# Optimization experiments

Measured on AMD Instinct MI355X. Metric: run time of the kernel, lower is better.

The kernel has to match this reference:

```python
import jax, jax.numpy as jnp
import numpy as np
import math

N_HEAD = 8
LN_EPS = 1e-5


def _layernorm(x, g, b):
    mu = jnp.mean(x, axis=-1, keepdims=True)
    var = jnp.mean(jnp.square(x - mu), axis=-1, keepdims=True)
    return (x - mu) / jnp.sqrt(var + LN_EPS) * g + b


def setup_inputs() -> dict:
    key0 = jax.random.key(0)
    ks = jax.random.split(key0, 12)
    B, L, D, E = 4, 512, 256, 5  # batch, agents, n_embd, edge_feats_dim

    def w(k, shape):
        return jax.random.normal(k, shape, dtype=jnp.float32) * 0.02

    return {
        "key": jax.random.normal(ks[0], (B, L, D), jnp.float32),
        "value": jax.random.normal(ks[1], (B, L, D), jnp.float32),
        "query": jax.random.normal(ks[2], (B, L, D), jnp.float32),
        "atten_masks": jax.random.randint(ks[3], (B, L, L), 0, 2).astype(jnp.int32),
        "edge_feats": jax.random.normal(ks[4], (B, L, L, E), jnp.float32),
        # Linear weights stored [in, out] so forward is x @ W + b
        "Wk": w(ks[5], (D, D)), "bk": jnp.zeros((D,), jnp.float32),
        "Wq": w(ks[6], (D, D)), "bq": jnp.zeros((D,), jnp.float32),
        "Wv": w(ks[7], (D, D)), "bv": jnp.zeros((D,), jnp.float32),
        "Wp": w(ks[8], (D, D)), "bp": jnp.zeros((D,), jnp.float32),
        "We1": w(ks[9], (E, D)), "be1": jnp.zeros((D,), jnp.float32),
        "ln_g": jnp.ones((D,), jnp.float32), "ln_b": jnp.zeros((D,), jnp.float32),
        "We2": w(ks[10], (D, N_HEAD)), "be2": jnp.zeros((N_HEAD,), jnp.float32),
    }


def reference(key, value, query, atten_masks, edge_feats,
              Wk, bk, Wq, bq, Wv, bv, Wp, bp,
              We1, be1, ln_g, ln_b, We2, be2):
    B, L, D = query.shape
    hd = D // N_HEAD
    # QKV projections -> [B, H, L, hd]
    q = (query @ Wq + bq).reshape(B, L, N_HEAD, hd).transpose(0, 2, 1, 3)
    k = (key @ Wk + bk).reshape(B, L, N_HEAD, hd).transpose(0, 2, 1, 3)
    v = (value @ Wv + bv).reshape(B, L, N_HEAD, hd).transpose(0, 2, 1, 3)
    # scaled attention scores [B, H, L, L]
    att = jnp.einsum('bhqd,bhkd->bhqk', q, k) * (1.0 / math.sqrt(hd))
    # edge-feature additive bias: Linear -> ReLU -> LayerNorm -> Linear(per-head)
    e = jax.nn.relu(edge_feats @ We1 + be1)          # [B, L, L, D]
    e = _layernorm(e, ln_g, ln_b)
    e = e @ We2 + be2                                # [B, L, L, H]
    att = att + e.transpose(0, 3, 1, 2)
    # additive mask (0 -> -inf), softmax over keys
    att = jnp.where(atten_masks[:, None, :, :] == 0, -jnp.inf, att)
    att = jax.nn.softmax(att, axis=-1)
    y = jnp.einsum('bhqk,bhkd->bhqd', att, v)        # [B, H, L, hd]
    y = y.transpose(0, 2, 1, 3).reshape(B, L, D)
    return y @ Wp + bp
```

## Files before the change

kernel.cpp:

```cpp
#include <hip/hip_runtime.h>
#include <hip/hip_bf16.h>

#define L_SEQ 512
#define D_EMB 256
#define NH 8
#define HD 32
#define LL (L_SEQ * L_SEQ)

typedef __attribute__((ext_vector_type(8))) short short8;
typedef __attribute__((ext_vector_type(4))) float f32x4;
typedef unsigned short ushort;

__device__ __forceinline__ float bf2f(ushort u) {
    unsigned int x = ((unsigned int)u) << 16;
    float f;
    __builtin_memcpy(&f, &x, 4);
    return f;
}
__device__ __forceinline__ ushort f2bf(float x) {
    __hip_bfloat16 h = __float2bfloat16(x);
    ushort u;
    __builtin_memcpy(&u, &h, 2);
    return u;
}
__device__ __forceinline__ unsigned int fbits(float x) {
    unsigned int u;
    __builtin_memcpy(&u, &x, 4);
    return u;
}
__device__ __forceinline__ float asf(unsigned int u) {
    float f;
    __builtin_memcpy(&f, &u, 4);
    return f;
}
__device__ __forceinline__ unsigned int pack_bf16rnd(float a, float b) {
    return __builtin_amdgcn_perm(fbits(b) + 0x8000u, fbits(a) + 0x8000u, 0x07060302u);
}
__device__ __forceinline__ unsigned int packhi(unsigned int y, unsigned int x) {
    return __builtin_amdgcn_perm(y, x, 0x07060302u);
}
__device__ __forceinline__ uint2 cvt_hilo2(float v0, float v1) {
    unsigned int hi = pack_bf16rnd(v0, v1);
    float h0 = asf(hi << 16);
    float h1 = asf(hi & 0xffff0000u);
    unsigned int lo = pack_bf16rnd(v0 - h0, v1 - h1);
    uint2 r; r.x = hi; r.y = lo;
    return r;
}

__global__ __launch_bounds__(256) void prep_kernel(
    const float* __restrict__ We1, const float* __restrict__ be1,
    const float* __restrict__ g,   const float* __restrict__ bta,
    const float* __restrict__ We2, const float* __restrict__ be2,
    const float* __restrict__ Wq, const float* __restrict__ Wk,
    const float* __restrict__ Wv, const float* __restrict__ Wp,
    ushort* __restrict__ W1G, ushort* __restrict__ B2G, float* __restrict__ tail,
    ushort* __restrict__ WThi, ushort* __restrict__ WTlo)
{
    int t = threadIdx.x;
    if (blockIdx.x != 0) {
        int bx = blockIdx.x - 1;
        int w = bx >> 4, ny = bx & 15;
        const float* W = (w == 0) ? Wq : (w == 1) ? Wk : (w == 2) ? Wv : Wp;
        ushort* dh = WThi + (size_t)w * 65536;
        ushort* dl = WTlo + (size_t)w * 65536;
        int n = ny * 16 + (t >> 4);
        int k0 = (t & 15) * 16;
        ushort hbuf[16], lbuf[16];
#pragma unroll
        for (int kk = 0; kk < 16; ++kk) {
            float v = W[(size_t)(k0 + kk) * 256 + n];
            unsigned int hb = fbits(v) + 0x8000u;
            ushort hi = (ushort)(hb >> 16);
            float res = v - bf2f(hi);
            hbuf[kk] = hi;
            lbuf[kk] = (ushort)((fbits(res) + 0x8000u) >> 16);
        }
        *(short8*)(dh + (size_t)n * 256 + k0)     = *(short8*)&hbuf[0];
        *(short8*)(dh + (size_t)n * 256 + k0 + 8) = *(short8*)&hbuf[8];
        *(short8*)(dl + (size_t)n * 256 + k0)     = *(short8*)&lbuf[0];
        *(short8*)(dl + (size_t)n * 256 + k0 + 8) = *(short8*)&lbuf[8];
        return;
    }

    __shared__ float red[16][256];
    float gd = g[t], bd = bta[t];
#pragma unroll
    for (int h = 0; h < 8; ++h) {
        float w2 = We2[t * 8 + h];
        red[h][t] = gd * w2;
        red[8 + h][t] = bd * w2;
    }
    __syncthreads();
    for (int off = 128; off > 0; off >>= 1) {
        if (t < off) {
#pragma unroll
            for (int row = 0; row < 16; ++row) red[row][t] += red[row][t + off];
        }
        __syncthreads();
    }
    if (t < 8) {
        tail[t] = red[t][0];
        tail[8 + t] = red[8 + t][0] + be2[t];
    }
    if (t >= 16 && t < 32) tail[t] = 0.f;

    for (int idx = t; idx < 8192; idx += 256) {
        int j = idx & 7, lane = (idx >> 3) & 63, tile = idx >> 9;
        int m = lane & 15, q = lane >> 4;
        int k = q * 8 + j;
        int d = (m >> 2) * 64 + tile * 4 + (m & 3);
        float v = 0.f;
        bool lo = false;
        if (k < 5)        v = We1[k * 256 + d];
        else if (k < 10)  { v = We1[(k - 5) * 256 + d]; lo = true; }
        else if (k < 15)  v = We1[(k - 10) * 256 + d];
        else if (k == 15) v = be1[d];
        else if (k == 16) { v = be1[d]; lo = true; }
        ushort hi = f2bf(v);
        W1G[idx] = lo ? f2bf(v - bf2f(hi)) : hi;
    }
    for (int idx = t; idx < 4096; idx += 256) {
        int j = idx & 7, lane = (idx >> 3) & 63, kc = idx >> 9;
        int n = lane & 15, q = lane >> 4;
        int d = kc * 32 + q * 8 + j;
        ushort out;
        if (n < 8)       out = f2bf(g[d] * We2[d * 8 + n]);
        else if (n == 8) out = 0x3F80;
        else             out = 0;
        B2G[idx] = out;
    }
}

__global__ __launch_bounds__(256) void gemm_mfma(
    const float* __restrict__ A0, const ushort* __restrict__ H0,
    const ushort* __restrict__ L0, const float* __restrict__ b0,
    float* __restrict__ C0, float* __restrict__ T0,
    const float* __restrict__ A1, const ushort* __restrict__ H1,
    const ushort* __restrict__ L1, const float* __restrict__ b1,
    float* __restrict__ C1, float* __restrict__ T1,
    const float* __restrict__ A2, const ushort* __restrict__ H2,
    const ushort* __restrict__ L2, const float* __restrict__ b2,
    float* __restrict__ C2, float* __restrict__ T2)
{
    const float* A; const ushort* BH; const ushort* BL;
    const float* bias; float* C; float* Ct;
    if (blockIdx.z == 0)      { A = A0; BH = H0; BL = L0; bias = b0; C = C0; Ct = T0; }
    else if (blockIdx.z == 1) { A = A1; BH = H1; BL = L1; bias = b1; C = C1; Ct = T1; }
    else                      { A = A2; BH = H2; BL = L2; bias = b2; C = C2; Ct = T2; }

    __shared__ ushort Ahi[64][40];
    __shared__ ushort Alo[64][40];

    int tid = threadIdx.x;
    int wv = tid >> 6, lane = tid & 63;
    int m = lane & 15, quad = lane >> 4;
    int bm = blockIdx.x * 64, bn = blockIdx.y * 64;

    int sm = tid >> 2, sg = (tid & 3) * 8;
    const float* Arow = A + (size_t)(bm + sm) * 256 + sg;

    int nrow = bn + wv * 16 + m;
    const ushort* bhp = BH + (size_t)nrow * 256 + quad * 8;
    const ushort* blp = BL + (size_t)nrow * 256 + quad * 8;

    f32x4 acc[4];
#pragma unroll
    for (int mt = 0; mt < 4; ++mt) acc[mt] = (f32x4){0.f, 0.f, 0.f, 0.f};

    for (int k0 = 0; k0 < 256; k0 += 32) {
        float4 a0 = *(const float4*)(Arow + k0);
        float4 a1 = *(const float4*)(Arow + k0 + 4);
        uint2 c0 = cvt_hilo2(a0.x, a0.y);
        uint2 c1 = cvt_hilo2(a0.z, a0.w);
        uint2 c2 = cvt_hilo2(a1.x, a1.y);
        uint2 c3 = cvt_hilo2(a1.z, a1.w);
        if (k0) __syncthreads();
        uint4 hq; hq.x = c0.x; hq.y = c1.x; hq.z = c2.x; hq.w = c3.x;
        uint4 lq; lq.x = c0.y; lq.y = c1.y; lq.z = c2.y; lq.w = c3.y;
        *(uint4*)&Ahi[sm][sg] = hq;
        *(uint4*)&Alo[sm][sg] = lq;
        __syncthreads();

        short8 bhi = *(const short8*)(bhp + k0);
        short8 blo = *(const short8*)(blp + k0);
#pragma unroll
        for (int mt = 0; mt < 4; ++mt) {
            short8 ahi = *(const short8*)&Ahi[mt * 16 + m][quad * 8];
            short8 alo = *(const short8*)&Alo[mt * 16 + m][quad * 8];
            acc[mt] = __builtin_amdgcn_mfma_f32_16x16x32_bf16(ahi, blo, acc[mt], 0, 0, 0);
            acc[mt] = __builtin_amdgcn_mfma_f32_16x16x32_bf16(alo, bhi, acc[mt], 0, 0, 0);
            acc[mt] = __builtin_amdgcn_mfma_f32_16x16x32_bf16(ahi, bhi, acc[mt], 0, 0, 0);
        }
    }

    float bn_bias = bias[nrow];
    if (Ct) {
        int bb = bm >> 9, l0 = bm & 511;
        float* outp = Ct + ((size_t)(bb * 256 + nrow)) * 512 + l0 + quad * 4;
#pragma unroll
        for (int mt = 0; mt < 4; ++mt) {
            float4 o;
            o.x = acc[mt][0] + bn_bias; o.y = acc[mt][1] + bn_bias;
            o.z = acc[mt][2] + bn_bias; o.w = acc[mt][3] + bn_bias;
            *(float4*)(outp + mt * 16) = o;
        }
    } else {
#pragma unroll
        for (int mt = 0; mt < 4; ++mt) {
#pragma unroll
            for (int r = 0; r < 4; ++r) {
                C[(size_t)(bm + mt * 16 + quad * 4 + r) * 256 + nrow] = acc[mt][r] + bn_bias;
            }
        }
    }
}

__global__ __launch_bounds__(256) void edge_bias_mfma(
    const float* __restrict__ EF, const ushort* __restrict__ W1G,
    const ushort* __restrict__ B2G, const float* __restrict__ tail,
    ushort* __restrict__ E2)
{
    __shared__ __align__(16) char xt[4 * 16 * 528];
    int tid = threadIdx.x;
    int wv = tid >> 6, lane = tid & 63;
    int q = lane >> 4, n = lane & 15;
    char* myx = xt + wv * (16 * 528);

    int bi = blockIdx.x;
    int b = bi >> 9, i = bi & 511;
    size_t rowbase = (size_t)bi * 512;

    short8 w1f[16];
#pragma unroll
    for (int t = 0; t < 16; ++t)
        w1f[t] = *(const short8*)(W1G + (t * 64 + lane) * 8);
    short8 b2f[8];
#pragma unroll
    for (int kc = 0; kc < 8; ++kc)
        b2f[kc] = *(const short8*)(B2G + (kc * 64 + lane) * 8);

    float shv = tail[n];
    float bbv = tail[8 + n];
    const float inv256 = 1.0f / 256.0f;

    const float* efbase = EF + rowbase * 5;
    int pairoff = wv * 16 + n;

    float4 evA = *(const float4*)(efbase + (size_t)pairoff * 5);
    float  evB = efbase[(size_t)pairoff * 5 + 4];

    for (int iter = 0; iter < 8; ++iter) {
        float4 nA; float nB;
        if (iter < 7) {
            const float* p = efbase + (size_t)((iter + 1) * 64 + pairoff) * 5;
            nA = *(const float4*)p;
            nB = p[4];
        }
        int jb = iter * 64 + wv * 16;

        unsigned int hb[5], la[5];
        hb[0] = fbits(evA.x); hb[1] = fbits(evA.y); hb[2] = fbits(evA.z);
        hb[3] = fbits(evA.w); hb[4] = fbits(evB);
        {
            float e0 = evA.x - asf(hb[0] & 0xffff0000u);
            float e1 = evA.y - asf(hb[1] & 0xffff0000u);
            float e2 = evA.z - asf(hb[2] & 0xffff0000u);
            float e3 = evA.w - asf(hb[3] & 0xffff0000u);
            float e4 = evB   - asf(hb[4] & 0xffff0000u);
            la[0] = fbits(e0) + 0x8000u;
            la[1] = fbits(e1) + 0x8000u;
            la[2] = fbits(e2) + 0x8000u;
            la[3] = fbits(e3) + 0x8000u;
            la[4] = fbits(e4) + 0x8000u;
        }
        unsigned int A0v = packhi(hb[1], hb[0]);
        unsigned int A1v = packhi(hb[3], hb[2]);
        unsigned int A2v = packhi(hb[0], hb[4]);
        unsigned int A3v = packhi(hb[2], hb[1]);
        unsigned int B0v = packhi(hb[4], hb[3]);
        unsigned int B1v = packhi(la[1], la[0]);
        unsigned int B2v = packhi(la[3], la[2]);
        unsigned int B3v = packhi(0x3F800000u, la[4]);
        uint4 efd;
        bool isq0 = (q == 0), isq1 = (q == 1), isq2 = (q == 2);
        efd.x = isq0 ? A0v : isq1 ? B0v : isq2 ? 0x3F80u : 0u;
        efd.y = isq0 ? A1v : isq1 ? B1v : 0u;
        efd.z = isq0 ? A2v : isq1 ? B2v : 0u;
        efd.w = isq0 ? A3v : isq1 ? B3v : 0u;
        short8 ef8;
        __builtin_memcpy(&ef8, &efd, 16);

        unsigned int pk0 = 0, pk1 = 0;
#pragma unroll
        for (int t = 0; t < 16; ++t) {
            f32x4 z = {0.f, 0.f, 0.f, 0.f};
            f32x4 d1 = __builtin_amdgcn_mfma_f32_16x16x32_bf16(w1f[t], ef8, z, 0, 0, 0);
            float x0 = fmaxf(d1[0], 0.f);
            float x1 = fmaxf(d1[1], 0.f);
            float x2 = fmaxf(d1[2], 0.f);
            float x3 = fmaxf(d1[3], 0.f);
            unsigned int pa = pack_bf16rnd(x0, x1);
            unsigned int pb = pack_bf16rnd(x2, x3);
            if (t & 1) {
                uint4 wq; wq.x = pk0; wq.y = pk1; wq.z = pa; wq.w = pb;
                *(uint4*)(myx + n * 528 + q * 128 + (t - 1) * 8) = wq;
            } else {
                pk0 = pa; pk1 = pb;
            }
        }

        f32x4 acc  = {0.f, 0.f, 0.f, 0.f};
        f32x4 acc2 = {0.f, 0.f, 0.f, 0.f};
#pragma unroll
        for (int kc = 0; kc < 8; ++kc) {
            short8 a = *(const short8*)(myx + n * 528 + kc * 64 + q * 16);
            acc  = __builtin_amdgcn_mfma_f32_16x16x32_bf16(a, b2f[kc], acc, 0, 0, 0);
            acc2 = __builtin_amdgcn_mfma_f32_16x16x32_bf16(a, a, acc2, 0, 0, 0);
        }

        int base = lane & 48;
        float er[4];
#pragma unroll
        for (int r = 0; r < 4; ++r) {
            float sm = __shfl(acc[r], base + 8);
            float sq = __shfl(acc2[r], base + (base >> 2) + r);
            float dot = acc[r];
            float mu = sm * inv256;
            float var = fmaf(-mu, mu, sq * inv256);
            float rs = rsqrtf(var + 1e-5f);
            er[r] = fmaf(dot - mu * shv, rs, bbv);
        }
        if (n < 8) {
            uint2 outv;
            outv.x = pack_bf16rnd(er[0], er[1]);
            outv.y = pack_bf16rnd(er[2], er[3]);
            size_t basep = (((size_t)(b * NH + n) * L_SEQ + i) * L_SEQ) + jb + q * 4;
            *(uint2*)(E2 + basep) = outv;
        }
        evA = nA; evB = nB;
    }
}

__global__ __launch_bounds__(256, 3) void attn_kernel(
    const float* __restrict__ Q, const float* __restrict__ Kt,
    const float* __restrict__ V, const ushort* __restrict__ E2,
    const int* __restrict__ MSK, float* __restrict__ Y)
{
    __shared__ float stage[4096];
    __shared__ float pbuf[4][4][520];
    __shared__ float qs_t[32][16];

    int bh = blockIdx.x;
    int b = bh >> 3, h = bh & 7;
    int tid = threadIdx.x;
    int wv = tid >> 6, lane = tid & 63;
    int i0 = blockIdx.y * 16;
    int i = i0 + wv * 4;

    const float* Ktb = Kt + (size_t)bh * (HD * L_SEQ);
    const float* Vb  = V + (size_t)b * L_SEQ * D_EMB + h * HD;

    size_t erow = ((size_t)bh * L_SEQ + i) * L_SEQ;
    size_t mrow = ((size_t)b * L_SEQ + i) * L_SEQ;

    unsigned int e2p[4][4];
    int2 mkp[4][4];
#pragma unroll
    for (int r = 0; r < 4; ++r)
#pragma unroll
        for (int c = 0; c < 4; ++c) {
            int j = c * 128 + 2 * lane;
            e2p[r][c] = *(const unsigned int*)(E2 + erow + (size_t)r * L_SEQ + j);
            mkp[r][c] = *(const int2*)(MSK + mrow + (size_t)r * L_SEQ + j);
        }

    if (tid < 128) {
        int r = tid >> 3, c4 = (tid & 7) * 4;
        float4 qv = *(const float4*)(Q + ((size_t)(b * L_SEQ + i0 + r)) * 256 + h * HD + c4);
        qs_t[c4 + 0][r] = qv.x; qs_t[c4 + 1][r] = qv.y;
        qs_t[c4 + 2][r] = qv.z; qs_t[c4 + 3][r] = qv.w;
    }

    float s[4][8];
#pragma unroll
    for (int r = 0; r < 4; ++r)
#pragma unroll
        for (int t = 0; t < 8; ++t) s[r][t] = 0.f;

    for (int c = 0; c < 4; ++c) {
        if (c) __syncthreads();
        {
            int d0 = tid >> 5, jj = (tid & 31) * 4;
#pragma unroll
            for (int p = 0; p < 4; ++p) {
                int d = p * 8 + d0;
                float4 kv = *(const float4*)(Ktb + (size_t)d * L_SEQ + c * 128 + jj);
                *(float4*)&stage[d * 128 + jj] = kv;
            }
        }
        __syncthreads();
        int c2 = c * 2;
#pragma unroll 8
        for (int d = 0; d < HD; ++d) {
            float4 q4 = *(const float4*)&qs_t[d][wv * 4];
            float2 kv = *(const float2*)&stage[d * 128 + 2 * lane];
            s[0][c2]     = fmaf(q4.x, kv.x, s[0][c2]);
            s[0][c2 + 1] = fmaf(q4.x, kv.y, s[0][c2 + 1]);
            s[1][c2]     = fmaf(q4.y, kv.x, s[1][c2]);
            s[1][c2 + 1] = fmaf(q4.y, kv.y, s[1][c2 + 1]);
            s[2][c2]     = fmaf(q4.z, kv.x, s[2][c2]);
            s[2][c2 + 1] = fmaf(q4.z, kv.y, s[2][c2 + 1]);
            s[3][c2]     = fmaf(q4.w, kv.x, s[3][c2]);
            s[3][c2 + 1] = fmaf(q4.w, kv.y, s[3][c2 + 1]);
        }
    }

    const float scl = 0.17677669529663687f;
#pragma unroll
    for (int r = 0; r < 4; ++r) {
        float sv[8];
        float m = -3.0e38f;
#pragma unroll
        for (int idx = 0; idx < 8; ++idx) {
            int c = idx >> 1, u = idx & 1;
            unsigned int pk = e2p[r][c];
            float e = bf2f((ushort)(u ? (pk >> 16) : (pk & 0xffff)));
            int mk = u ? mkp[r][c].y : mkp[r][c].x;
            float v = (mk != 0) ? fmaf(s[r][idx], scl, e) : -1e30f;
            sv[idx] = v;
            m = fmaxf(m, v);
        }
#pragma unroll
        for (int o = 32; o > 0; o >>= 1) m = fmaxf(m, __shfl_xor(m, o));
        float ssum = 0.f;
#pragma unroll
        for (int idx = 0; idx < 8; ++idx) {
            float p = __expf(sv[idx] - m);
            sv[idx] = p;
            ssum += p;
        }
#pragma unroll
        for (int o = 32; o > 0; o >>= 1) ssum += __shfl_xor(ssum, o);
        float inv = 1.0f / ssum;
#pragma unroll
        for (int c = 0; c < 4; ++c) {
            float2 w;
            w.x = sv[c * 2] * inv;
            w.y = sv[c * 2 + 1] * inv;
            *(float2*)&pbuf[wv][r][c * 128 + 2 * lane] = w;
        }
    }

    int dg = lane >> 3, js = lane & 7;
    float4 acc[4];
#pragma unroll
    for (int r = 0; r < 4; ++r) { acc[r].x = 0.f; acc[r].y = 0.f; acc[r].z = 0.f; acc[r].w = 0.f; }

    for (int c = 0; c < 4; ++c) {
        __syncthreads();
        {
            int j0 = tid >> 3, dd = (tid & 7) * 4;
#pragma unroll
            for (int p = 0; p < 4; ++p) {
                int j = p * 32 + j0;
                float4 vv = *(const float4*)(Vb + (size_t)(c * 128 + j) * D_EMB + dd);
                *(float4*)&stage[j * 32 + dd] = vv;
            }
        }
        __syncthreads();
#pragma unroll
        for (int jb = 0; jb < 16; ++jb) {
            int jj = jb * 8 + js;
            float4 v4 = *(const float4*)&stage[jj * 32 + dg * 4];
#pragma unroll
            for (int r = 0; r < 4; ++r) {
                float p = pbuf[wv][r][c * 128 + jj];
                acc[r].x = fmaf(p, v4.x, acc[r].x);
                acc[r].y = fmaf(p, v4.y, acc[r].y);
                acc[r].z = fmaf(p, v4.z, acc[r].z);
                acc[r].w = fmaf(p, v4.w, acc[r].w);
            }
        }
    }

#pragma unroll
    for (int off = 1; off < 8; off <<= 1) {
#pragma unroll
        for (int r = 0; r < 4; ++r) {
            acc[r].x += __shfl_xor(acc[r].x, off);
            acc[r].y += __shfl_xor(acc[r].y, off);
            acc[r].z += __shfl_xor(acc[r].z, off);
            acc[r].w += __shfl_xor(acc[r].w, off);
        }
    }
    if (js == 0) {
#pragma unroll
        for (int r = 0; r < 4; ++r)
            *(float4*)(Y + ((size_t)(b * L_SEQ + i + r)) * 256 + h * HD + dg * 4) = acc[r];
    }
}

extern "C" void kernel_launch(void* const* d_in, const int* in_sizes, int n_in,
                              void* d_out, int out_size, void* d_ws, size_t ws_size,
                              hipStream_t stream)
{
    const float* key   = (const float*)d_in[0];
    const float* value = (const float*)d_in[1];
    const float* query = (const float*)d_in[2];
    const int*   msk   = (const int*)d_in[3];
    const float* ef    = (const float*)d_in[4];
    const float* Wk  = (const float*)d_in[5];  const float* bk  = (const float*)d_in[6];
    const float* Wq  = (const float*)d_in[7];  const float* bq  = (const float*)d_in[8];
    const float* Wv  = (const float*)d_in[9];  const float* bv  = (const float*)d_in[10];
    const float* Wp  = (const float*)d_in[11]; const float* bp  = (const float*)d_in[12];
    const float* We1 = (const float*)d_in[13]; const float* be1 = (const float*)d_in[14];
    const float* lng = (const float*)d_in[15]; const float* lnb = (const float*)d_in[16];
    const float* We2 = (const float*)d_in[17]; const float* be2 = (const float*)d_in[18];

    const int MTOK = 4 * L_SEQ;
    const int NELT = MTOK * D_EMB;

    float* ws    = (float*)d_ws;
    float* Qw    = ws;
    float* Vw    = Qw + NELT;
    float* Yw    = Vw + NELT;
    float* Ktw   = Yw + NELT;
    ushort* W1G  = (ushort*)(Ktw + NELT);
    ushort* B2G  = W1G + 8192;
    float* tail  = (float*)(B2G + 4096);
    ushort* WThi = (ushort*)(tail + 32);
    ushort* WTlo = WThi + 4 * 65536;
    ushort* E2   = WTlo + 4 * 65536;

    hipLaunchKernelGGL(prep_kernel, dim3(65), dim3(256), 0, stream,
                       We1, be1, lng, lnb, We2, be2,
                       Wq, Wk, Wv, Wp,
                       W1G, B2G, tail, WThi, WTlo);
    hipLaunchKernelGGL(gemm_mfma, dim3(32, 4, 3), dim3(256), 0, stream,
                       query, WThi + 0 * 65536, WTlo + 0 * 65536, bq, Qw,  (float*)nullptr,
                       key,   WThi + 1 * 65536, WTlo + 1 * 65536, bk, (float*)nullptr, Ktw,
                       value, WThi + 2 * 65536, WTlo + 2 * 65536, bv, Vw,  (float*)nullptr);
    hipLaunchKernelGGL(edge_bias_mfma, dim3(2048), dim3(256), 0, stream,
                       ef, W1G, B2G, tail, E2);
    hipLaunchKernelGGL(attn_kernel, dim3(32, 32), dim3(256), 0, stream,
                       Qw, Ktw, Vw, E2, msk, Yw);
    hipLaunchKernelGGL(gemm_mfma, dim3(32, 4, 1), dim3(256), 0, stream,
                       Yw, WThi + 3 * 65536, WTlo + 3 * 65536, bp, (float*)d_out, (float*)nullptr,
                       Yw, WThi + 3 * 65536, WTlo + 3 * 65536, bp, (float*)d_out, (float*)nullptr,
                       Yw, WThi + 3 * 65536, WTlo + 3 * 65536, bp, (float*)d_out, (float*)nullptr);
}
```

Baseline: 228.5 us.

## Software-pipeline edge bias kernel with double-buffered LDS stage

```diff
diff --git a/kernel.cpp b/kernel.cpp
--- a/kernel.cpp
+++ b/kernel.cpp
@@ -216,16 +216,72 @@
     }
 }
 
+__device__ __forceinline__ void edge_stage_a(
+    const short8* w1f, float4 evA, float evB, int q, int n, char* dst)
+{
+    unsigned int hb[5], la[5];
+    hb[0] = fbits(evA.x); hb[1] = fbits(evA.y); hb[2] = fbits(evA.z);
+    hb[3] = fbits(evA.w); hb[4] = fbits(evB);
+    {
+        float e0 = evA.x - asf(hb[0] & 0xffff0000u);
+        float e1 = evA.y - asf(hb[1] & 0xffff0000u);
+        float e2 = evA.z - asf(hb[2] & 0xffff0000u);
+        float e3 = evA.w - asf(hb[3] & 0xffff0000u);
+        float e4 = evB   - asf(hb[4] & 0xffff0000u);
+        la[0] = fbits(e0) + 0x8000u;
+        la[1] = fbits(e1) + 0x8000u;
+        la[2] = fbits(e2) + 0x8000u;
+        la[3] = fbits(e3) + 0x8000u;
+        la[4] = fbits(e4) + 0x8000u;
+    }
+    unsigned int A0v = packhi(hb[1], hb[0]);
+    unsigned int A1v = packhi(hb[3], hb[2]);
+    unsigned int A2v = packhi(hb[0], hb[4]);
+    unsigned int A3v = packhi(hb[2], hb[1]);
+    unsigned int B0v = packhi(hb[4], hb[3]);
+    unsigned int B1v = packhi(la[1], la[0]);
+    unsigned int B2v = packhi(la[3], la[2]);
+    unsigned int B3v = packhi(0x3F800000u, la[4]);
+    uint4 efd;
+    bool isq0 = (q == 0), isq1 = (q == 1), isq2 = (q == 2);
+    efd.x = isq0 ? A0v : isq1 ? B0v : isq2 ? 0x3F80u : 0u;
+    efd.y = isq0 ? A1v : isq1 ? B1v : 0u;
+    efd.z = isq0 ? A2v : isq1 ? B2v : 0u;
+    efd.w = isq0 ? A3v : isq1 ? B3v : 0u;
+    short8 ef8;
+    __builtin_memcpy(&ef8, &efd, 16);
+
+    unsigned int pk0 = 0, pk1 = 0;
+#pragma unroll
+    for (int t = 0; t < 16; ++t) {
+        f32x4 z = {0.f, 0.f, 0.f, 0.f};
+        f32x4 d1 = __builtin_amdgcn_mfma_f32_16x16x32_bf16(w1f[t], ef8, z, 0, 0, 0);
+        float x0 = fmaxf(d1[0], 0.f);
+        float x1 = fmaxf(d1[1], 0.f);
+        float x2 = fmaxf(d1[2], 0.f);
+        float x3 = fmaxf(d1[3], 0.f);
+        unsigned int pa = pack_bf16rnd(x0, x1);
+        unsigned int pb = pack_bf16rnd(x2, x3);
+        if (t & 1) {
+            uint4 wq; wq.x = pk0; wq.y = pk1; wq.z = pa; wq.w = pb;
+            *(uint4*)(dst + n * 528 + q * 128 + (t - 1) * 8) = wq;
+        } else {
+            pk0 = pa; pk1 = pb;
+        }
+    }
+}
+
 __global__ __launch_bounds__(256) void edge_bias_mfma(
     const float* __restrict__ EF, const ushort* __restrict__ W1G,
     const ushort* __restrict__ B2G, const float* __restrict__ tail,
     ushort* __restrict__ E2)
 {
-    __shared__ __align__(16) char xt[4 * 16 * 528];
+    __shared__ __align__(16) char xt[2 * 4 * 16 * 528];
     int tid = threadIdx.x;
     int wv = tid >> 6, lane = tid & 63;
     int q = lane >> 4, n = lane & 15;
-    char* myx = xt + wv * (16 * 528);
+    char* xb0 = xt + wv * (16 * 528);
+    char* xb1 = xt + 33792 + wv * (16 * 528);
 
     int bi = blockIdx.x;
     int b = bi >> 9, i = bi & 511;
@@ -247,78 +303,44 @@
     const float* efbase = EF + rowbase * 5;
     int pairoff = wv * 16 + n;
 
-    float4 evA = *(const float4*)(efbase + (size_t)pairoff * 5);
-    float  evB = efbase[(size_t)pairoff * 5 + 4];
+    float4 e0A = *(const float4*)(efbase + (size_t)pairoff * 5);
+    float  e0B = efbase[(size_t)pairoff * 5 + 4];
+    edge_stage_a(w1f, e0A, e0B, q, n, xb0);
+
+    float4 evA1; float evB1;
+    {
+        const float* p = efbase + (size_t)(64 + pairoff) * 5;
+        evA1 = *(const float4*)p;
+        evB1 = p[4];
+    }
 
     for (int iter = 0; iter < 8; ++iter) {
-        float4 nA; float nB;
-        if (iter < 7) {
-            const float* p = efbase + (size_t)((iter + 1) * 64 + pairoff) * 5;
-            nA = *(const float4*)p;
-            nB = p[4];
-        }
+        float4 nxA; float nxB;
+        if (iter < 6) {
+            const float* p = efbase + (size_t)((iter + 2) * 64 + pairoff) * 5;
+            nxA = *(const float4*)p;
+            nxB = p[4];
+        }
+        if (iter < 7)
+            edge_stage_a(w1f, evA1, evB1, q, n, ((iter + 1) & 1) ? xb1 : xb0);
+
+        char* xr = (iter & 1) ? xb1 : xb0;
+        f32x4 aA = {0.f, 0.f, 0.f, 0.f}, aB = {0.f, 0.f, 0.f, 0.f};
+        f32x4 sA = {0.f, 0.f, 0.f, 0.f}, sB = {0.f, 0.f, 0.f, 0.f};
+#pragma unroll
+        for (int kc = 0; kc < 8; kc += 2) {
+            short8 a0 = *(const short8*)(xr + n * 528 + kc * 64 + q * 16);
+            short8 a1 = *(const short8*)(xr + n * 528 + (kc + 1) * 64 + q * 16);
+            aA = __builtin_amdgcn_mfma_f32_16x16x32_bf16(a0, b2f[kc], aA, 0, 0, 0);
+            sA = __builtin_amdgcn_mfma_f32_16x16x32_bf16(a0, a0, sA, 0, 0, 0);
+            aB = __builtin_amdgcn_mfma_f32_16x16x32_bf16(a1, b2f[kc + 1], aB, 0, 0, 0);
+            sB = __builtin_amdgcn_mfma_f32_16x16x32_bf16(a1, a1, sB, 0, 0, 0);
+        }
+        f32x4 acc, acc2;
+#pragma unroll
+        for (int r = 0; r < 4; ++r) { acc[r] = aA[r] + aB[r]; acc2[r] = sA[r] + sB[r]; }
+
         int jb = iter * 64 + wv * 16;
-
-        unsigned int hb[5], la[5];
-        hb[0] = fbits(evA.x); hb[1] = fbits(evA.y); hb[2] = fbits(evA.z);
-        hb[3] = fbits(evA.w); hb[4] = fbits(evB);
-        {
-            float e0 = evA.x - asf(hb[0] & 0xffff0000u);
-            float e1 = evA.y - asf(hb[1] & 0xffff0000u);
-            float e2 = evA.z - asf(hb[2] & 0xffff0000u);
-            float e3 = evA.w - asf(hb[3] & 0xffff0000u);
-            float e4 = evB   - asf(hb[4] & 0xffff0000u);
-            la[0] = fbits(e0) + 0x8000u;
-            la[1] = fbits(e1) + 0x8000u;
-            la[2] = fbits(e2) + 0x8000u;
-            la[3] = fbits(e3) + 0x8000u;
-            la[4] = fbits(e4) + 0x8000u;
-        }
-        unsigned int A0v = packhi(hb[1], hb[0]);
-        unsigned int A1v = packhi(hb[3], hb[2]);
-        unsigned int A2v = packhi(hb[0], hb[4]);
-        unsigned int A3v = packhi(hb[2], hb[1]);
-        unsigned int B0v = packhi(hb[4], hb[3]);
-        unsigned int B1v = packhi(la[1], la[0]);
-        unsigned int B2v = packhi(la[3], la[2]);
-        unsigned int B3v = packhi(0x3F800000u, la[4]);
-        uint4 efd;
-        bool isq0 = (q == 0), isq1 = (q == 1), isq2 = (q == 2);
-        efd.x = isq0 ? A0v : isq1 ? B0v : isq2 ? 0x3F80u : 0u;
-        efd.y = isq0 ? A1v : isq1 ? B1v : 0u;
-        efd.z = isq0 ? A2v : isq1 ? B2v : 0u;
-        efd.w = isq0 ? A3v : isq1 ? B3v : 0u;
-        short8 ef8;
-        __builtin_memcpy(&ef8, &efd, 16);
-
-        unsigned int pk0 = 0, pk1 = 0;
-#pragma unroll
-        for (int t = 0; t < 16; ++t) {
-            f32x4 z = {0.f, 0.f, 0.f, 0.f};
-            f32x4 d1 = __builtin_amdgcn_mfma_f32_16x16x32_bf16(w1f[t], ef8, z, 0, 0, 0);
-            float x0 = fmaxf(d1[0], 0.f);
-            float x1 = fmaxf(d1[1], 0.f);
-            float x2 = fmaxf(d1[2], 0.f);
-            float x3 = fmaxf(d1[3], 0.f);
-            unsigned int pa = pack_bf16rnd(x0, x1);
-            unsigned int pb = pack_bf16rnd(x2, x3);
-            if (t & 1) {
-                uint4 wq; wq.x = pk0; wq.y = pk1; wq.z = pa; wq.w = pb;
-                *(uint4*)(myx + n * 528 + q * 128 + (t - 1) * 8) = wq;
-            } else {
-                pk0 = pa; pk1 = pb;
-            }
-        }
-
-        f32x4 acc  = {0.f, 0.f, 0.f, 0.f};
-        f32x4 acc2 = {0.f, 0.f, 0.f, 0.f};
-#pragma unroll
-        for (int kc = 0; kc < 8; ++kc) {
-            short8 a = *(const short8*)(myx + n * 528 + kc * 64 + q * 16);
-            acc  = __builtin_amdgcn_mfma_f32_16x16x32_bf16(a, b2f[kc], acc, 0, 0, 0);
-            acc2 = __builtin_amdgcn_mfma_f32_16x16x32_bf16(a, a, acc2, 0, 0, 0);
-        }
-
         int base = lane & 48;
         float er[4];
 #pragma unroll
@@ -338,7 +360,7 @@
             size_t basep = (((size_t)(b * NH + n) * L_SEQ + i) * L_SEQ) + jb + q * 4;
             *(uint2*)(E2 + basep) = outv;
         }
-        evA = nA; evB = nB;
+        evA1 = nxA; evB1 = nxB;
     }
 }
 
```

New measurement: 237.8 us. 4.1% more time.

## Store softmax probs as bf16 interleaved by row, read Q via scalar loads

Applied to the files above, without the earlier changes.

```diff
diff --git a/kernel.cpp b/kernel.cpp
--- a/kernel.cpp
+++ b/kernel.cpp
@@ -342,14 +342,13 @@
     }
 }
 
-__global__ __launch_bounds__(256, 3) void attn_kernel(
+__global__ __launch_bounds__(256, 4) void attn_kernel(
     const float* __restrict__ Q, const float* __restrict__ Kt,
     const float* __restrict__ V, const ushort* __restrict__ E2,
     const int* __restrict__ MSK, float* __restrict__ Y)
 {
     __shared__ float stage[4096];
-    __shared__ float pbuf[4][4][520];
-    __shared__ float qs_t[32][16];
+    __shared__ ushort pbuf[4][512][4];
 
     int bh = blockIdx.x;
     int b = bh >> 3, h = bh & 7;
@@ -361,6 +360,9 @@
     const float* Ktb = Kt + (size_t)bh * (HD * L_SEQ);
     const float* Vb  = V + (size_t)b * L_SEQ * D_EMB + h * HD;
 
+    int wvu = __builtin_amdgcn_readfirstlane(wv);
+    const float* Qs = Q + ((size_t)(b * L_SEQ + i0 + wvu * 4)) * 256 + h * HD;
+
     size_t erow = ((size_t)bh * L_SEQ + i) * L_SEQ;
     size_t mrow = ((size_t)b * L_SEQ + i) * L_SEQ;
 
@@ -374,13 +376,6 @@
             e2p[r][c] = *(const unsigned int*)(E2 + erow + (size_t)r * L_SEQ + j);
             mkp[r][c] = *(const int2*)(MSK + mrow + (size_t)r * L_SEQ + j);
         }
-
-    if (tid < 128) {
-        int r = tid >> 3, c4 = (tid & 7) * 4;
-        float4 qv = *(const float4*)(Q + ((size_t)(b * L_SEQ + i0 + r)) * 256 + h * HD + c4);
-        qs_t[c4 + 0][r] = qv.x; qs_t[c4 + 1][r] = qv.y;
-        qs_t[c4 + 2][r] = qv.z; qs_t[c4 + 3][r] = qv.w;
-    }
 
     float s[4][8];
 #pragma unroll
@@ -401,25 +396,27 @@
         }
         __syncthreads();
         int c2 = c * 2;
-#pragma unroll 8
+#pragma unroll
         for (int d = 0; d < HD; ++d) {
-            float4 q4 = *(const float4*)&qs_t[d][wv * 4];
+            float q0 = Qs[0 * 256 + d];
+            float q1 = Qs[1 * 256 + d];
+            float q2 = Qs[2 * 256 + d];
+            float q3 = Qs[3 * 256 + d];
             float2 kv = *(const float2*)&stage[d * 128 + 2 * lane];
-            s[0][c2]     = fmaf(q4.x, kv.x, s[0][c2]);
-            s[0][c2 + 1] = fmaf(q4.x, kv.y, s[0][c2 + 1]);
-            s[1][c2]     = fmaf(q4.y, kv.x, s[1][c2]);
-            s[1][c2 + 1] = fmaf(q4.y, kv.y, s[1][c2 + 1]);
-            s[2][c2]     = fmaf(q4.z, kv.x, s[2][c2]);
-            s[2][c2 + 1] = fmaf(q4.z, kv.y, s[2][c2 + 1]);
-            s[3][c2]     = fmaf(q4.w, kv.x, s[3][c2]);
-            s[3][c2 + 1] = fmaf(q4.w, kv.y, s[3][c2 + 1]);
+            s[0][c2]     = fmaf(q0, kv.x, s[0][c2]);
+            s[0][c2 + 1] = fmaf(q0, kv.y, s[0][c2 + 1]);
+            s[1][c2]     = fmaf(q1, kv.x, s[1][c2]);
+            s[1][c2 + 1] = fmaf(q1, kv.y, s[1][c2 + 1]);
+            s[2][c2]     = fmaf(q2, kv.x, s[2][c2]);
+            s[2][c2 + 1] = fmaf(q2, kv.y, s[2][c2 + 1]);
+            s[3][c2]     = fmaf(q3, kv.x, s[3][c2]);
+            s[3][c2 + 1] = fmaf(q3, kv.y, s[3][c2 + 1]);
         }
     }
 
     const float scl = 0.17677669529663687f;
 #pragma unroll
     for (int r = 0; r < 4; ++r) {
-        float sv[8];
         float m = -3.0e38f;
 #pragma unroll
         for (int idx = 0; idx < 8; ++idx) {
@@ -428,7 +425,7 @@
             float e = bf2f((ushort)(u ? (pk >> 16) : (pk & 0xffff)));
             int mk = u ? mkp[r][c].y : mkp[r][c].x;
             float v = (mk != 0) ? fmaf(s[r][idx], scl, e) : -1e30f;
-            sv[idx] = v;
+            s[r][idx] = v;
             m = fmaxf(m, v);
         }
 #pragma unroll
@@ -436,20 +433,25 @@
         float ssum = 0.f;
 #pragma unroll
         for (int idx = 0; idx < 8; ++idx) {
-            float p = __expf(sv[idx] - m);
-            sv[idx] = p;
+            float p = __expf(s[r][idx] - m);
+            s[r][idx] = p;
             ssum += p;
         }
 #pragma unroll
         for (int o = 32; o > 0; o >>= 1) ssum += __shfl_xor(ssum, o);
         float inv = 1.0f / ssum;
 #pragma unroll
-        for (int c = 0; c < 4; ++c) {
-            float2 w;
-            w.x = sv[c * 2] * inv;
-            w.y = sv[c * 2 + 1] * inv;
-            *(float2*)&pbuf[wv][r][c * 128 + 2 * lane] = w;
-        }
+        for (int idx = 0; idx < 8; ++idx) s[r][idx] *= inv;
+    }
+#pragma unroll
+    for (int c = 0; c < 4; ++c) {
+        int c2 = c * 2;
+        uint4 w;
+        w.x = pack_bf16rnd(s[0][c2],     s[1][c2]);
+        w.y = pack_bf16rnd(s[2][c2],     s[3][c2]);
+        w.z = pack_bf16rnd(s[0][c2 + 1], s[1][c2 + 1]);
+        w.w = pack_bf16rnd(s[2][c2 + 1], s[3][c2 + 1]);
+        *(uint4*)&pbuf[wv][c * 128 + 2 * lane][0] = w;
     }
 
     int dg = lane >> 3, js = lane & 7;
@@ -473,14 +475,27 @@
         for (int jb = 0; jb < 16; ++jb) {
             int jj = jb * 8 + js;
             float4 v4 = *(const float4*)&stage[jj * 32 + dg * 4];
-#pragma unroll
-            for (int r = 0; r < 4; ++r) {
-                float p = pbuf[wv][r][c * 128 + jj];
-                acc[r].x = fmaf(p, v4.x, acc[r].x);
-                acc[r].y = fmaf(p, v4.y, acc[r].y);
-                acc[r].z = fmaf(p, v4.z, acc[r].z);
-                acc[r].w = fmaf(p, v4.w, acc[r].w);
-            }
+            uint2 pu = *(const uint2*)&pbuf[wv][c * 128 + jj][0];
+            float p0 = asf(pu.x << 16);
+            float p1 = asf(pu.x & 0xffff0000u);
+            float p2 = asf(pu.y << 16);
+            float p3 = asf(pu.y & 0xffff0000u);
+            acc[0].x = fmaf(p0, v4.x, acc[0].x);
+            acc[0].y = fmaf(p0, v4.y, acc[0].y);
+            acc[0].z = fmaf(p0, v4.z, acc[0].z);
+            acc[0].w = fmaf(p0, v4.w, acc[0].w);
+            acc[1].x = fmaf(p1, v4.x, acc[1].x);
+            acc[1].y = fmaf(p1, v4.y, acc[1].y);
+            acc[1].z = fmaf(p1, v4.z, acc[1].z);
+            acc[1].w = fmaf(p1, v4.w, acc[1].w);
+            acc[2].x = fmaf(p2, v4.x, acc[2].x);
+            acc[2].y = fmaf(p2, v4.y, acc[2].y);
+            acc[2].z = fmaf(p2, v4.z, acc[2].z);
+            acc[2].w = fmaf(p2, v4.w, acc[2].w);
+            acc[3].x = fmaf(p3, v4.x, acc[3].x);
+            acc[3].y = fmaf(p3, v4.y, acc[3].y);
+            acc[3].z = fmaf(p3, v4.z, acc[3].z);
+            acc[3].w = fmaf(p3, v4.w, acc[3].w);
         }
     }
 
```

Measured after the change: 225.8 us. No clear change (-1.2%).
